# Optimization experiments

Hardware: AMD Instinct MI355X
Metric: run time of the kernel (lower is better)

## Reference

```python
import jax, jax.numpy as jnp
import numpy as np

TEMPERATURE = 0.07
BASE_TEMPERATURE = 0.07
NUM_HEADS = 4


def setup_inputs() -> dict:
    key = jax.random.key(0)
    k1, k2 = jax.random.split(key)
    features = jax.random.normal(k1, (2048, 2, 256), dtype=jnp.float32)
    labels = jax.random.randint(k2, (2048, 10), 0, 2).astype(jnp.float32)
    return {"features": features, "labels": labels}


def reference(features, labels):
    B, V, E = features.shape
    H = NUM_HEADS
    fs = E // H
    N = B * V

    # torch.cat(torch.unbind(features, dim=1), dim=0): view-major stacking
    f = jnp.transpose(features, (1, 0, 2)).reshape(N, H, fs)
    # F.normalize(dim=-1) with eps=1e-12 clamp
    norm = jnp.sqrt(jnp.sum(f * f, axis=-1, keepdims=True))
    f = f / jnp.maximum(norm, 1e-12)

    # per-head pairwise similarities: dot[i, j, h] = <f[i,h], f[j,h]>  (N, N, H)
    dot = jnp.einsum('ihf,jhf->ijh', f, f)
    heads = jnp.argmax(dot, axis=-1)              # (N, N) head chosen per (anchor, positive)
    dotT = dot / TEMPERATURE

    # logits_max is over j for fixed (i, head); detached in the original
    maxh = jax.lax.stop_gradient(jnp.max(dotT, axis=1))   # (N, H)

    # positive mask, tiled across views, self removed
    mask = (labels @ labels.T) > 0                # (B, B) bool
    mask = jnp.tile(mask, (V, V)).astype(f.dtype)  # (N, N)
    logits_mask = 1.0 - jnp.eye(N, dtype=f.dtype)  # (N, N)
    mask = mask * logits_mask

    # masked exp-sum per (anchor, head): S[i,h] = sum_j lm[i,j] * exp(dotT[i,j,h] - maxh[i,h])
    exp_l = jnp.exp(dotT - maxh[:, None, :])       # (N, N, H)
    S = jnp.einsum('ij,ijh->ih', logits_mask, exp_l)  # (N, H)
    logS = jnp.log(S)

    # select per-pair head: log_prob[i,k] = dotT[i,k,h(i,k)] - maxh[i,h(i,k)] - logS[i,h(i,k)]
    dot_sel = jnp.take_along_axis(dotT, heads[..., None], axis=2)[..., 0]  # (N, N)
    max_sel = jnp.take_along_axis(maxh, heads, axis=1)                     # (N, N)
    logS_sel = jnp.take_along_axis(logS, heads, axis=1)                    # (N, N)
    log_prob = dot_sel - max_sel - logS_sel

    mean_log_prob_pos = jnp.sum(mask * log_prob, axis=1) / jnp.sum(mask, axis=1)
    loss = -(TEMPERATURE / BASE_TEMPERATURE) * mean_log_prob_pos

    finite = jnp.isfinite(loss)
    return jnp.sum(jnp.where(finite, loss, 0.0)) / jnp.sum(finite)
```

## Files before the change

### kernel.cpp

```cpp
#include <hip/hip_runtime.h>
#include <math.h>

#define BS    2048
#define NROW  4096
#define EDIM  256
#define LDSW  264
#define INVT  (1.0f/0.07f)

typedef float  float4v __attribute__((ext_vector_type(4)));
typedef short  short8v __attribute__((ext_vector_type(8)));

static __device__ __forceinline__ unsigned short f2bf(float x) {
    unsigned u = __builtin_bit_cast(unsigned, x);
    u += 0x7fffu + ((u >> 16) & 1u);
    return (unsigned short)(u >> 16);
}

__global__ void lab_kernel(const float* __restrict__ labels, unsigned* __restrict__ bits) {
    int i = blockIdx.x * blockDim.x + threadIdx.x;
    if (i < BS) {
        unsigned b = 0;
#pragma unroll
        for (int d = 0; d < 10; ++d)
            b |= (labels[i * 10 + d] != 0.0f ? 1u : 0u) << d;
        bits[i] = b;
    }
}

__global__ void norm_kernel(const float* __restrict__ feat, unsigned short* __restrict__ fnb) {
    int i = blockIdx.x;
    int t = threadIdx.x;
    int b = i & (BS - 1);
    int v = i >> 11;
    float x = feat[(size_t)b * (2 * EDIM) + (size_t)v * EDIM + t];
    float ss = x * x;
#pragma unroll
    for (int off = 32; off > 0; off >>= 1)
        ss += __shfl_xor(ss, off, 64);
    float nrm = fmaxf(sqrtf(ss), 1e-12f);
    fnb[(size_t)i * EDIM + t] = f2bf(x / nrm);
}

__global__ __launch_bounds__(256, 2) void main_kernel(
    const unsigned short* __restrict__ fnb, const unsigned* __restrict__ bits,
    float* __restrict__ S, float* __restrict__ Num, float* __restrict__ Cnt) {

    __shared__ unsigned short shB[64 * LDSW];

    const int tid  = threadIdx.x;
    const int lane = tid & 63;
    const int wave = tid >> 6;
    const int quad = lane >> 4;
    const int ml   = lane & 15;
    const int i0   = blockIdx.x * 64;
    const int jc0  = blockIdx.y * 512;
    const int wi   = (wave >> 1) * 32;
    const int wj   = (wave & 1) * 32;
    const float MSH = INVT;

    short8v af[2][4][2];
#pragma unroll
    for (int is = 0; is < 2; ++is) {
        const unsigned short* ap = fnb + (size_t)(i0 + wi + is * 16 + ml) * EDIM + quad * 8;
#pragma unroll
        for (int h = 0; h < 4; ++h)
#pragma unroll
            for (int kk = 0; kk < 2; ++kk)
                af[is][h][kk] = *(const short8v*)(ap + h * 64 + kk * 32);
    }

    unsigned ibr[8];
#pragma unroll
    for (int p = 0; p < 8; ++p)
        ibr[p] = bits[(i0 + wi + (p >> 2) * 16 + quad * 4 + (p & 3)) & (BS - 1)];

    float Sp[8][4] = {};
    float np[8] = {};
    int   cpk[8] = {};

    for (int t = 0; t < 8; ++t) {
        const int j0 = jc0 + t * 64;
        __syncthreads();
#pragma unroll
        for (int q = 0; q < 8; ++q) {
            int s = tid + 256 * q;
            int r = s >> 5, c = (s & 31) * 8;
            *(uint4*)(shB + r * LDSW + c) = *(const uint4*)(fnb + (size_t)(j0 + r) * EDIM + c);
        }
        __syncthreads();

        const unsigned jb0 = bits[(j0 + wj + ml) & (BS - 1)];
        const unsigned jb1 = bits[(j0 + wj + 16 + ml) & (BS - 1)];

        float4v dacc[2][2][4];
#pragma unroll
        for (int a = 0; a < 2; ++a)
#pragma unroll
            for (int b = 0; b < 2; ++b)
#pragma unroll
                for (int h = 0; h < 4; ++h)
                    dacc[a][b][h] = (float4v){0.f, 0.f, 0.f, 0.f};

#pragma unroll
        for (int h = 0; h < 4; ++h)
#pragma unroll
            for (int kk = 0; kk < 2; ++kk) {
                const int ko = h * 64 + kk * 32 + quad * 8;
                short8v b0 = *(const short8v*)(shB + (wj + ml) * LDSW + ko);
                short8v b1 = *(const short8v*)(shB + (wj + 16 + ml) * LDSW + ko);
                dacc[0][0][h] = __builtin_amdgcn_mfma_f32_16x16x32_bf16(af[0][h][kk], b0, dacc[0][0][h], 0, 0, 0);
                dacc[0][1][h] = __builtin_amdgcn_mfma_f32_16x16x32_bf16(af[0][h][kk], b1, dacc[0][1][h], 0, 0, 0);
                dacc[1][0][h] = __builtin_amdgcn_mfma_f32_16x16x32_bf16(af[1][h][kk], b0, dacc[1][0][h], 0, 0, 0);
                dacc[1][1][h] = __builtin_amdgcn_mfma_f32_16x16x32_bf16(af[1][h][kk], b1, dacc[1][1][h], 0, 0, 0);
            }

#pragma unroll
        for (int is = 0; is < 2; ++is)
#pragma unroll
            for (int r = 0; r < 4; ++r) {
                const int p = is * 4 + r;
                const int i = i0 + wi + is * 16 + quad * 4 + r;
                const unsigned ibit = ibr[p];
#pragma unroll
                for (int js = 0; js < 2; ++js) {
                    const int j = j0 + wj + js * 16 + ml;
                    const unsigned jbit = js ? jb1 : jb0;
                    const float d0 = dacc[is][js][0][r];
                    const float d1 = dacc[is][js][1][r];
                    const float d2 = dacc[is][js][2][r];
                    const float d3 = dacc[is][js][3][r];
                    float bd = d0; int bh = 0;
                    if (d1 > bd) { bd = d1; bh = 1; }
                    if (d2 > bd) { bd = d2; bh = 2; }
                    if (d3 > bd) { bd = d3; bh = 3; }
                    const bool off = (i != j);
                    const float e0 = __expf(fmaf(d0, INVT, -MSH));
                    const float e1 = __expf(fmaf(d1, INVT, -MSH));
                    const float e2 = __expf(fmaf(d2, INVT, -MSH));
                    const float e3 = __expf(fmaf(d3, INVT, -MSH));
                    if (off) {
                        Sp[p][0] += e0; Sp[p][1] += e1; Sp[p][2] += e2; Sp[p][3] += e3;
                    }
                    if (off && (ibit & jbit)) {
                        np[p] += bd;
                        cpk[p] += 1 << (bh * 8);
                    }
                }
            }
    }

#pragma unroll
    for (int p = 0; p < 8; ++p) {
        const int i = i0 + wi + (p >> 2) * 16 + quad * 4 + (p & 3);
        float v[9];
        v[0] = np[p];
#pragma unroll
        for (int h = 0; h < 4; ++h) v[1 + h] = Sp[p][h];
#pragma unroll
        for (int h = 0; h < 4; ++h) v[5 + h] = (float)((cpk[p] >> (8 * h)) & 255);
#pragma unroll
        for (int k = 0; k < 9; ++k) {
            float x = v[k];
            x += __shfl_xor(x, 1, 64);
            x += __shfl_xor(x, 2, 64);
            x += __shfl_xor(x, 4, 64);
            x += __shfl_xor(x, 8, 64);
            v[k] = x;
        }
        if (ml == 0) {
            atomicAdd(&Num[i], v[0] * INVT);
#pragma unroll
            for (int h = 0; h < 4; ++h) atomicAdd(&S[i * 4 + h], v[1 + h]);
#pragma unroll
            for (int h = 0; h < 4; ++h) atomicAdd(&Cnt[i * 4 + h], v[5 + h]);
        }
    }
}

__global__ void final_kernel(const float* __restrict__ S, const float* __restrict__ Num,
                             const float* __restrict__ Cnt, float* __restrict__ out) {
    const float MSH = INVT;
    int tid = threadIdx.x;
    float ls = 0.f, lc = 0.f;
    for (int i = tid; i < NROW; i += 1024) {
        float c = 0.f;
        float numr = Num[i];
#pragma unroll
        for (int h = 0; h < 4; ++h) {
            float sh = S[i * 4 + h];
            float ch = Cnt[i * 4 + h];
            numr -= ch * (MSH + logf(sh));
            c += ch;
        }
        if (c > 0.f) { ls += -(numr / c); lc += 1.f; }
    }
    __shared__ float rs[1024], rc[1024];
    rs[tid] = ls; rc[tid] = lc;
    __syncthreads();
    for (int s = 512; s > 0; s >>= 1) {
        if (tid < s) { rs[tid] += rs[tid + s]; rc[tid] += rc[tid + s]; }
        __syncthreads();
    }
    if (tid == 0) out[0] = rs[0] / rc[0];
}

extern "C" void kernel_launch(void* const* d_in, const int* in_sizes, int n_in,
                              void* d_out, int out_size, void* d_ws, size_t ws_size,
                              hipStream_t stream) {
    const float* feat = (const float*)d_in[0];
    const float* labels = (const float*)d_in[1];
    float* out = (float*)d_out;

    char* ws = (char*)d_ws;
    unsigned short* fnb = (unsigned short*)ws;
    float* S = (float*)(ws + (size_t)NROW * EDIM * sizeof(unsigned short));
    float* Num = S + NROW * 4;
    float* Cnt = Num + NROW;
    unsigned* bits = (unsigned*)(Cnt + NROW * 4);

    hipMemsetAsync(S, 0, (size_t)NROW * 9 * sizeof(float), stream);

    lab_kernel<<<8, 256, 0, stream>>>(labels, bits);
    norm_kernel<<<NROW, 256, 0, stream>>>(feat, fnb);
    main_kernel<<<dim3(64, 8), 256, 0, stream>>>(fnb, bits, S, Num, Cnt);
    final_kernel<<<1, 1024, 0, stream>>>(S, Num, Cnt, out);
}
```

Measured before the change: 126.5 us.

## Fuse prep kernels, retile main kernel with swizzled direct-to-LDS loads, parallelize final

Merges label packing, normalization and accumulator zeroing into one prep kernel, which removes the memset and a launch. The main kernel now gives each wave 16 rows against 64 columns, doubles the grid in j, and raises occupancy to 3 blocks per CU. It loads B tiles with global_load_lds using an XOR swizzle in place of a padded LDS layout. The final reduction is spread over 16 blocks with atomics and a completion counter, at the cost of more atomics and less A-fragment reuse per wave.

```diff
diff --git a/kernel.cpp b/kernel.cpp
--- a/kernel.cpp
+++ b/kernel.cpp
@@ -4,7 +4,6 @@
 #define BS    2048
 #define NROW  4096
 #define EDIM  256
-#define LDSW  264
 #define INVT  (1.0f/0.07f)
 
 typedef float  float4v __attribute__((ext_vector_type(4)));
@@ -16,148 +15,147 @@
     return (unsigned short)(u >> 16);
 }
 
-__global__ void lab_kernel(const float* __restrict__ labels, unsigned* __restrict__ bits) {
-    int i = blockIdx.x * blockDim.x + threadIdx.x;
-    if (i < BS) {
-        unsigned b = 0;
+static __device__ __forceinline__ void gload_lds16(const void* g, void* l) {
+    __builtin_amdgcn_global_load_lds(
+        (const __attribute__((address_space(1))) unsigned int*)g,
+        (__attribute__((address_space(3))) unsigned int*)l, 16, 0, 0);
+}
+
+__global__ void prep_kernel(const float* __restrict__ feat, const float* __restrict__ labels,
+                            unsigned short* __restrict__ fnb, unsigned* __restrict__ bits,
+                            float* __restrict__ zacc) {
+    const int b = blockIdx.x, t = threadIdx.x;
+    if (b < NROW) {
+        int bb = b & (BS - 1);
+        int v = b >> 11;
+        float x = feat[(size_t)bb * (2 * EDIM) + (size_t)v * EDIM + t];
+        float ss = x * x;
+#pragma unroll
+        for (int off = 32; off > 0; off >>= 1)
+            ss += __shfl_xor(ss, off, 64);
+        float nrm = fmaxf(sqrtf(ss), 1e-12f);
+        fnb[(size_t)b * EDIM + t] = f2bf(x / nrm);
+    } else {
+        int g = (b - NROW) * 256 + t;
+        unsigned bb = 0;
 #pragma unroll
         for (int d = 0; d < 10; ++d)
-            b |= (labels[i * 10 + d] != 0.0f ? 1u : 0u) << d;
-        bits[i] = b;
-    }
-}
-
-__global__ void norm_kernel(const float* __restrict__ feat, unsigned short* __restrict__ fnb) {
-    int i = blockIdx.x;
-    int t = threadIdx.x;
-    int b = i & (BS - 1);
-    int v = i >> 11;
-    float x = feat[(size_t)b * (2 * EDIM) + (size_t)v * EDIM + t];
-    float ss = x * x;
-#pragma unroll
-    for (int off = 32; off > 0; off >>= 1)
-        ss += __shfl_xor(ss, off, 64);
-    float nrm = fmaxf(sqrtf(ss), 1e-12f);
-    fnb[(size_t)i * EDIM + t] = f2bf(x / nrm);
-}
-
-__global__ __launch_bounds__(256, 2) void main_kernel(
+            bb |= (labels[g * 10 + d] != 0.0f ? 1u : 0u) << d;
+        bits[g] = bb;
+        for (int k = g; k < NROW * 9 + 3; k += 2048) zacc[k] = 0.0f;
+    }
+}
+
+__global__ __launch_bounds__(256, 3) void main_kernel(
     const unsigned short* __restrict__ fnb, const unsigned* __restrict__ bits,
     float* __restrict__ S, float* __restrict__ Num, float* __restrict__ Cnt) {
 
-    __shared__ unsigned short shB[64 * LDSW];
+    __shared__ unsigned short shB[64 * 256];
 
     const int tid  = threadIdx.x;
     const int lane = tid & 63;
     const int wave = tid >> 6;
     const int quad = lane >> 4;
     const int ml   = lane & 15;
-    const int i0   = blockIdx.x * 64;
-    const int jc0  = blockIdx.y * 512;
-    const int wi   = (wave >> 1) * 32;
-    const int wj   = (wave & 1) * 32;
-    const float MSH = INVT;
-
-    short8v af[2][4][2];
-#pragma unroll
-    for (int is = 0; is < 2; ++is) {
-        const unsigned short* ap = fnb + (size_t)(i0 + wi + is * 16 + ml) * EDIM + quad * 8;
+    const int xr   = ml & 7;
+    const int i0   = blockIdx.x * 64 + wave * 16;
+    const int jc0  = blockIdx.y * 256;
+
+    short8v af[4][2];
+    {
+        const unsigned short* ap = fnb + (size_t)(i0 + ml) * EDIM + quad * 8;
 #pragma unroll
         for (int h = 0; h < 4; ++h)
 #pragma unroll
             for (int kk = 0; kk < 2; ++kk)
-                af[is][h][kk] = *(const short8v*)(ap + h * 64 + kk * 32);
-    }
-
-    unsigned ibr[8];
-#pragma unroll
-    for (int p = 0; p < 8; ++p)
-        ibr[p] = bits[(i0 + wi + (p >> 2) * 16 + quad * 4 + (p & 3)) & (BS - 1)];
-
-    float Sp[8][4] = {};
-    float np[8] = {};
-    int   cpk[8] = {};
-
-    for (int t = 0; t < 8; ++t) {
+                af[h][kk] = *(const short8v*)(ap + h * 64 + kk * 32);
+    }
+
+    unsigned ibr[4];
+#pragma unroll
+    for (int r = 0; r < 4; ++r)
+        ibr[r] = bits[(i0 + quad * 4 + r) & (BS - 1)];
+
+    float    Sp[4][4] = {};
+    float    np[4] = {};
+    unsigned cpk[4] = {};
+
+    for (int t = 0; t < 4; ++t) {
         const int j0 = jc0 + t * 64;
         __syncthreads();
 #pragma unroll
         for (int q = 0; q < 8; ++q) {
-            int s = tid + 256 * q;
-            int r = s >> 5, c = (s & 31) * 8;
-            *(uint4*)(shB + r * LDSW + c) = *(const uint4*)(fnb + (size_t)(j0 + r) * EDIM + c);
+            const int G   = tid + 256 * q;
+            const int row = G >> 5;
+            const int gg  = (G & 31) ^ (row & 7);
+            gload_lds16(fnb + (size_t)(j0 + row) * EDIM + gg * 8, shB + G * 8);
         }
         __syncthreads();
 
-        const unsigned jb0 = bits[(j0 + wj + ml) & (BS - 1)];
-        const unsigned jb1 = bits[(j0 + wj + 16 + ml) & (BS - 1)];
-
-        float4v dacc[2][2][4];
-#pragma unroll
-        for (int a = 0; a < 2; ++a)
-#pragma unroll
-            for (int b = 0; b < 2; ++b)
-#pragma unroll
-                for (int h = 0; h < 4; ++h)
-                    dacc[a][b][h] = (float4v){0.f, 0.f, 0.f, 0.f};
+        unsigned jbr[4];
+#pragma unroll
+        for (int js = 0; js < 4; ++js)
+            jbr[js] = bits[(j0 + js * 16 + ml) & (BS - 1)];
+
+        float4v dacc[4][4];
+#pragma unroll
+        for (int js = 0; js < 4; ++js)
+#pragma unroll
+            for (int h = 0; h < 4; ++h)
+                dacc[js][h] = (float4v){0.f, 0.f, 0.f, 0.f};
 
 #pragma unroll
         for (int h = 0; h < 4; ++h)
 #pragma unroll
             for (int kk = 0; kk < 2; ++kk) {
-                const int ko = h * 64 + kk * 32 + quad * 8;
-                short8v b0 = *(const short8v*)(shB + (wj + ml) * LDSW + ko);
-                short8v b1 = *(const short8v*)(shB + (wj + 16 + ml) * LDSW + ko);
-                dacc[0][0][h] = __builtin_amdgcn_mfma_f32_16x16x32_bf16(af[0][h][kk], b0, dacc[0][0][h], 0, 0, 0);
-                dacc[0][1][h] = __builtin_amdgcn_mfma_f32_16x16x32_bf16(af[0][h][kk], b1, dacc[0][1][h], 0, 0, 0);
-                dacc[1][0][h] = __builtin_amdgcn_mfma_f32_16x16x32_bf16(af[1][h][kk], b0, dacc[1][0][h], 0, 0, 0);
-                dacc[1][1][h] = __builtin_amdgcn_mfma_f32_16x16x32_bf16(af[1][h][kk], b1, dacc[1][1][h], 0, 0, 0);
-            }
-
-#pragma unroll
-        for (int is = 0; is < 2; ++is)
-#pragma unroll
-            for (int r = 0; r < 4; ++r) {
-                const int p = is * 4 + r;
-                const int i = i0 + wi + is * 16 + quad * 4 + r;
-                const unsigned ibit = ibr[p];
-#pragma unroll
-                for (int js = 0; js < 2; ++js) {
-                    const int j = j0 + wj + js * 16 + ml;
-                    const unsigned jbit = js ? jb1 : jb0;
-                    const float d0 = dacc[is][js][0][r];
-                    const float d1 = dacc[is][js][1][r];
-                    const float d2 = dacc[is][js][2][r];
-                    const float d3 = dacc[is][js][3][r];
-                    float bd = d0; int bh = 0;
-                    if (d1 > bd) { bd = d1; bh = 1; }
-                    if (d2 > bd) { bd = d2; bh = 2; }
-                    if (d3 > bd) { bd = d3; bh = 3; }
-                    const bool off = (i != j);
-                    const float e0 = __expf(fmaf(d0, INVT, -MSH));
-                    const float e1 = __expf(fmaf(d1, INVT, -MSH));
-                    const float e2 = __expf(fmaf(d2, INVT, -MSH));
-                    const float e3 = __expf(fmaf(d3, INVT, -MSH));
-                    if (off) {
-                        Sp[p][0] += e0; Sp[p][1] += e1; Sp[p][2] += e2; Sp[p][3] += e3;
-                    }
-                    if (off && (ibit & jbit)) {
-                        np[p] += bd;
-                        cpk[p] += 1 << (bh * 8);
-                    }
+                const int gsw = ((h * 8 + kk * 4 + quad) ^ xr) * 8;
+#pragma unroll
+                for (int js = 0; js < 4; ++js) {
+                    short8v bf = *(const short8v*)(shB + (js * 16 + ml) * 256 + gsw);
+                    dacc[js][h] = __builtin_amdgcn_mfma_f32_16x16x32_bf16(af[h][kk], bf, dacc[js][h], 0, 0, 0);
                 }
             }
-    }
-
-#pragma unroll
-    for (int p = 0; p < 8; ++p) {
-        const int i = i0 + wi + (p >> 2) * 16 + quad * 4 + (p & 3);
+
+#pragma unroll
+        for (int r = 0; r < 4; ++r) {
+            const int i = i0 + quad * 4 + r;
+            const unsigned ibit = ibr[r];
+#pragma unroll
+            for (int js = 0; js < 4; ++js) {
+                const int j = j0 + js * 16 + ml;
+                const float d0 = dacc[js][0][r];
+                const float d1 = dacc[js][1][r];
+                const float d2 = dacc[js][2][r];
+                const float d3 = dacc[js][3][r];
+                float bd = d0; int bh = 0;
+                if (d1 > bd) { bd = d1; bh = 1; }
+                if (d2 > bd) { bd = d2; bh = 2; }
+                if (d3 > bd) { bd = d3; bh = 3; }
+                const bool off = (i != j);
+                const float e0 = __expf(fmaf(d0, INVT, -INVT));
+                const float e1 = __expf(fmaf(d1, INVT, -INVT));
+                const float e2 = __expf(fmaf(d2, INVT, -INVT));
+                const float e3 = __expf(fmaf(d3, INVT, -INVT));
+                if (off) {
+                    Sp[r][0] += e0; Sp[r][1] += e1; Sp[r][2] += e2; Sp[r][3] += e3;
+                }
+                if (off && (ibit & jbr[js])) {
+                    np[r] += bd;
+                    cpk[r] += 1u << (bh * 8);
+                }
+            }
+        }
+    }
+
+#pragma unroll
+    for (int r = 0; r < 4; ++r) {
+        const int i = i0 + quad * 4 + r;
         float v[9];
-        v[0] = np[p];
-#pragma unroll
-        for (int h = 0; h < 4; ++h) v[1 + h] = Sp[p][h];
-#pragma unroll
-        for (int h = 0; h < 4; ++h) v[5 + h] = (float)((cpk[p] >> (8 * h)) & 255);
+        v[0] = np[r];
+#pragma unroll
+        for (int h = 0; h < 4; ++h) v[1 + h] = Sp[r][h];
+#pragma unroll
+        for (int h = 0; h < 4; ++h) v[5 + h] = (float)((cpk[r] >> (8 * h)) & 255u);
 #pragma unroll
         for (int k = 0; k < 9; ++k) {
             float x = v[k];
@@ -178,30 +176,39 @@
 }
 
 __global__ void final_kernel(const float* __restrict__ S, const float* __restrict__ Num,
-                             const float* __restrict__ Cnt, float* __restrict__ out) {
-    const float MSH = INVT;
-    int tid = threadIdx.x;
+                             const float* __restrict__ Cnt, float* __restrict__ red,
+                             unsigned* __restrict__ done, float* __restrict__ out) {
+    const int tid = threadIdx.x;
+    const int i = blockIdx.x * 256 + tid;
+    float c = 0.f;
+    float numr = Num[i];
+#pragma unroll
+    for (int h = 0; h < 4; ++h) {
+        float sh = S[i * 4 + h];
+        float ch = Cnt[i * 4 + h];
+        numr -= ch * (INVT + logf(sh));
+        c += ch;
+    }
     float ls = 0.f, lc = 0.f;
-    for (int i = tid; i < NROW; i += 1024) {
-        float c = 0.f;
-        float numr = Num[i];
-#pragma unroll
-        for (int h = 0; h < 4; ++h) {
-            float sh = S[i * 4 + h];
-            float ch = Cnt[i * 4 + h];
-            numr -= ch * (MSH + logf(sh));
-            c += ch;
-        }
-        if (c > 0.f) { ls += -(numr / c); lc += 1.f; }
-    }
-    __shared__ float rs[1024], rc[1024];
+    if (c > 0.f) { ls = -(numr / c); lc = 1.f; }
+
+    __shared__ float rs[256], rc[256];
     rs[tid] = ls; rc[tid] = lc;
     __syncthreads();
-    for (int s = 512; s > 0; s >>= 1) {
+    for (int s = 128; s > 0; s >>= 1) {
         if (tid < s) { rs[tid] += rs[tid + s]; rc[tid] += rc[tid + s]; }
         __syncthreads();
     }
-    if (tid == 0) out[0] = rs[0] / rc[0];
+    if (tid == 0) {
+        atomicAdd(&red[0], rs[0]);
+        atomicAdd(&red[1], rc[0]);
+        __threadfence();
+        if (atomicAdd(done, 1u) == 15u) {
+            float s = atomicAdd(&red[0], 0.0f);
+            float cc = atomicAdd(&red[1], 0.0f);
+            out[0] = s / cc;
+        }
+    }
 }
 
 extern "C" void kernel_launch(void* const* d_in, const int* in_sizes, int n_in,
@@ -216,12 +223,11 @@
     float* S = (float*)(ws + (size_t)NROW * EDIM * sizeof(unsigned short));
     float* Num = S + NROW * 4;
     float* Cnt = Num + NROW;
-    unsigned* bits = (unsigned*)(Cnt + NROW * 4);
-
-    hipMemsetAsync(S, 0, (size_t)NROW * 9 * sizeof(float), stream);
-
-    lab_kernel<<<8, 256, 0, stream>>>(labels, bits);
-    norm_kernel<<<NROW, 256, 0, stream>>>(feat, fnb);
-    main_kernel<<<dim3(64, 8), 256, 0, stream>>>(fnb, bits, S, Num, Cnt);
-    final_kernel<<<1, 1024, 0, stream>>>(S, Num, Cnt, out);
-}
+    float* red = Cnt + NROW * 4;
+    unsigned* done = (unsigned*)(red + 2);
+    unsigned* bits = done + 1;
+
+    prep_kernel<<<NROW + 8, 256, 0, stream>>>(feat, labels, fnb, bits, S);
+    main_kernel<<<dim3(64, 16), 256, 0, stream>>>(fnb, bits, S, Num, Cnt);
+    final_kernel<<<16, 256, 0, stream>>>(S, Num, Cnt, red, done, out);
+}
```

Result: faster. 116.6 us (-7.8%).
